# Performance work log

Measured on AMD Instinct MI355X. Metric: run time of the kernel, lower is better.

The kernel has to match this reference:

```python
import jax, jax.numpy as jnp
import numpy as np

D_MODEL = 1024
NUM_HEADS = 16
D_K = D_MODEL // NUM_HEADS
B, T = 2, 2048


def setup_inputs() -> dict:
    key = jax.random.key(0)
    k1, k2, k3 = jax.random.split(key, 3)
    scale = 1.0 / np.sqrt(D_MODEL)
    return {
        "x": jax.random.normal(k1, (B, T, D_MODEL), dtype=jnp.float32),
        "Wqkv": jax.random.normal(k2, (D_MODEL, 3 * D_MODEL), dtype=jnp.float32) * scale,
        "bqkv": jnp.zeros((3 * D_MODEL,), dtype=jnp.float32),
        "Wout": jax.random.normal(k3, (D_MODEL, D_MODEL), dtype=jnp.float32) * scale,
        "bout": jnp.zeros((D_MODEL,), dtype=jnp.float32),
    }


def reference(x, Wqkv, bqkv, Wout, bout):
    b, t, c = x.shape
    h, dk = NUM_HEADS, D_K
    qkv = x @ Wqkv + bqkv                      # [B,T,3C]
    q, k, v = jnp.split(qkv, 3, axis=-1)       # each [B,T,C]

    def split_heads(u):
        return u.reshape(b, t, h, dk).transpose(0, 2, 1, 3)  # [B,H,T,dk]

    q, k, v = split_heads(q), split_heads(k), split_heads(v)
    scores = jnp.einsum("bhqd,bhkd->bhqk", q, k) / jnp.sqrt(jnp.float32(dk))
    causal = jnp.tril(jnp.ones((t, t), dtype=bool))          # True = keep
    scores = jnp.where(causal, scores, -jnp.inf)
    attn = jax.nn.softmax(scores, axis=-1)
    out = jnp.einsum("bhqk,bhkd->bhqd", attn, v)             # [B,H,T,dk]
    concat = out.transpose(0, 2, 1, 3).reshape(b, t, c)
    return concat @ Wout + bout
```

## Files before the change

kernel.cpp:

```cpp
#include <hip/hip_runtime.h>
#include <hip/hip_bf16.h>

#define DEVI __device__ __forceinline__

typedef __attribute__((ext_vector_type(8))) short bf16x8;
typedef __attribute__((ext_vector_type(4))) float f32x4;

DEVI void load_lds16(const void* g, void* l) {
  __builtin_amdgcn_global_load_lds((const __attribute__((address_space(1))) void*)g,
                                   (__attribute__((address_space(3))) void*)l, 16, 0, 0);
}

DEVI short f32_to_bf16_bits(float f) {
  __hip_bfloat16 b = __float2bfloat16(f);
  return __builtin_bit_cast(short, b);
}

__global__ __launch_bounds__(256) void cvt_bf16_kernel(
    const float* __restrict__ in, __hip_bfloat16* __restrict__ out, int n4) {
  int i = blockIdx.x * 256 + threadIdx.x;
  if (i < n4) {
    float4 v = ((const float4*)in)[i];
    ushort4 o;
    o.x = (unsigned short)f32_to_bf16_bits(v.x);
    o.y = (unsigned short)f32_to_bf16_bits(v.y);
    o.z = (unsigned short)f32_to_bf16_bits(v.z);
    o.w = (unsigned short)f32_to_bf16_bits(v.w);
    ((ushort4*)out)[i] = o;
  }
}

__global__ __launch_bounds__(256) void transpose_bf16_kernel(
    const float* __restrict__ in, __hip_bfloat16* __restrict__ out, int K, int N) {
  __shared__ float tile[32][33];
  int tx = threadIdx.x, ty = threadIdx.y;
  int bx = blockIdx.x, by = blockIdx.y;
#pragma unroll
  for (int i = 0; i < 4; ++i) {
    int k = by * 32 + ty + i * 8;
    int n = bx * 32 + tx;
    tile[ty + i * 8][tx] = in[(size_t)k * N + n];
  }
  __syncthreads();
#pragma unroll
  for (int i = 0; i < 4; ++i) {
    int n = bx * 32 + ty + i * 8;
    int k = by * 32 + tx;
    out[(size_t)n * K + k] = __float2bfloat16(tile[tx][ty + i * 8]);
  }
}

template <int MODE>
__global__ __launch_bounds__(256) void gemm_bt_kernel(
    const __hip_bfloat16* __restrict__ A, const __hip_bfloat16* __restrict__ Bt,
    const float* __restrict__ bias, void* __restrict__ Cout,
    unsigned short* __restrict__ vt, int M, int N, int K) {
  __shared__ short As[128 * 64];
  __shared__ short Bs[128 * 64];
  const int tid = threadIdx.x;
  const int wid = tid >> 6, lane = tid & 63;
  const int bm = blockIdx.y, bn = blockIdx.x;
  const int row0 = bm * 128, col0 = bn * 128;
  const int wr = wid >> 1, wc = wid & 1;
  f32x4 acc[4][4] = {};

  for (int kt = 0; kt < K; kt += 64) {
    __syncthreads();
#pragma unroll
    for (int c = 0; c < 4; ++c) {
      int r = wid * 32 + c * 8 + (lane >> 3);
      int ss = (lane & 7) ^ (r & 7);
      load_lds16(A + (size_t)(row0 + r) * K + kt + ss * 8, As + (wid * 32 + c * 8) * 64);
      load_lds16(Bt + (size_t)(col0 + r) * K + kt + ss * 8, Bs + (wid * 32 + c * 8) * 64);
    }
    __syncthreads();
#pragma unroll
    for (int ks = 0; ks < 2; ++ks) {
      bf16x8 af[4], bf[4];
#pragma unroll
      for (int mi = 0; mi < 4; ++mi) {
        int r = wr * 64 + mi * 16 + (lane & 15);
        int sl = (ks * 4 + (lane >> 4)) ^ (r & 7);
        af[mi] = *(const bf16x8*)(As + r * 64 + sl * 8);
      }
#pragma unroll
      for (int ni = 0; ni < 4; ++ni) {
        int r = wc * 64 + ni * 16 + (lane & 15);
        int sl = (ks * 4 + (lane >> 4)) ^ (r & 7);
        bf[ni] = *(const bf16x8*)(Bs + r * 64 + sl * 8);
      }
#pragma unroll
      for (int mi = 0; mi < 4; ++mi)
#pragma unroll
        for (int ni = 0; ni < 4; ++ni)
          acc[mi][ni] = __builtin_amdgcn_mfma_f32_16x16x32_bf16(af[mi], bf[ni], acc[mi][ni], 0, 0, 0);
    }
  }
  const int crow0 = row0 + wr * 64, ccol0 = col0 + wc * 64;
#pragma unroll
  for (int ni = 0; ni < 4; ++ni) {
    int cc = ccol0 + ni * 16 + (lane & 15);
    float bv = bias[cc];
    if (MODE == 2 && cc >= 2048) {
      int dcol = cc - 2048;
      int hh = dcol >> 6, dl = dcol & 63;
#pragma unroll
      for (int mi = 0; mi < 4; ++mi) {
        int rr0 = crow0 + mi * 16 + (lane >> 4) * 4;
        int bI = rr0 >> 11, t0 = rr0 & 2047;
        ushort4 pk;
        pk.x = (unsigned short)f32_to_bf16_bits(acc[mi][ni][0] + bv);
        pk.y = (unsigned short)f32_to_bf16_bits(acc[mi][ni][1] + bv);
        pk.z = (unsigned short)f32_to_bf16_bits(acc[mi][ni][2] + bv);
        pk.w = (unsigned short)f32_to_bf16_bits(acc[mi][ni][3] + bv);
        *(ushort4*)(vt + ((size_t)(bI * 16 + hh) * 64 + dl) * 2048 + t0) = pk;
      }
    } else {
#pragma unroll
      for (int mi = 0; mi < 4; ++mi) {
#pragma unroll
        for (int r = 0; r < 4; ++r) {
          int rr = crow0 + mi * 16 + (lane >> 4) * 4 + r;
          float v = acc[mi][ni][r] + bv;
          if (MODE == 2)
            ((__hip_bfloat16*)Cout)[(size_t)rr * 2048 + cc] = __float2bfloat16(v);
          else
            ((float*)Cout)[(size_t)rr * N + cc] = v;
        }
      }
    }
  }
}

__global__ __launch_bounds__(256) void attn_kernel(
    const __hip_bfloat16* __restrict__ qk, const __hip_bfloat16* __restrict__ vt,
    __hip_bfloat16* __restrict__ concat) {
  const int bh = blockIdx.x;
  const int qb = blockIdx.y;
  const int b = bh >> 4, h = bh & 15;
  const int tid = threadIdx.x, wid = tid >> 6, lane = tid & 63;
  const size_t RS = 2048;
  const __hip_bfloat16* Qb = qk + (size_t)b * 2048 * RS + h * 64;
  const __hip_bfloat16* Kb = Qb + 1024;
  const __hip_bfloat16* Vh = vt + (size_t)bh * 64 * 2048;

  __shared__ short Ks[2][64 * 64];
  __shared__ short Vs[2][64 * 64];
  __shared__ short Ps[4][16 * 64];

  bf16x8 qf[2];
#pragma unroll
  for (int s = 0; s < 2; ++s)
    qf[s] = *(const bf16x8*)(Qb + (size_t)(qb * 64 + wid * 16 + (lane & 15)) * RS + s * 32 + (lane >> 4) * 8);

  f32x4 oacc[4] = {};
  float m_r[4], l_r[4];
#pragma unroll
  for (int r = 0; r < 4; ++r) { m_r[r] = -__builtin_inff(); l_r[r] = 0.f; }

#pragma unroll
  for (int c = 0; c < 2; ++c) {
    int r = wid * 16 + c * 8 + (lane >> 3);
    int ss = (lane & 7) ^ (r & 7);
    load_lds16(Kb + (size_t)r * RS + ss * 8, &Ks[0][(wid * 16 + c * 8) * 64]);
    load_lds16(Vh + (size_t)r * 2048 + ss * 8, &Vs[0][(wid * 16 + c * 8) * 64]);
  }
  int cur = 0;
  const float cs = 0.18033688f;

  for (int kt = 0; kt <= qb; ++kt) {
    __syncthreads();
    if (kt < qb) {
      int kn = kt + 1;
#pragma unroll
      for (int c = 0; c < 2; ++c) {
        int r = wid * 16 + c * 8 + (lane >> 3);
        int ss = (lane & 7) ^ (r & 7);
        load_lds16(Kb + (size_t)(kn * 64 + r) * RS + ss * 8, &Ks[cur ^ 1][(wid * 16 + c * 8) * 64]);
        load_lds16(Vh + (size_t)r * 2048 + kn * 64 + ss * 8, &Vs[cur ^ 1][(wid * 16 + c * 8) * 64]);
      }
    }

    f32x4 sacc[4] = {};
#pragma unroll
    for (int s = 0; s < 2; ++s) {
#pragma unroll
      for (int nt = 0; nt < 4; ++nt) {
        int r = nt * 16 + (lane & 15);
        int sl = (s * 4 + (lane >> 4)) ^ (r & 7);
        bf16x8 kf = *(const bf16x8*)(&Ks[cur][r * 64 + sl * 8]);
        sacc[nt] = __builtin_amdgcn_mfma_f32_16x16x32_bf16(qf[s], kf, sacc[nt], 0, 0, 0);
      }
    }

    const bool diag = (kt == qb);
#pragma unroll
    for (int r = 0; r < 4; ++r) {
      int qg = wid * 16 + (lane >> 4) * 4 + r;
      float rm = -3.0e38f;
#pragma unroll
      for (int nt = 0; nt < 4; ++nt) {
        float v = sacc[nt][r] * cs;
        if (diag) {
          int kg = nt * 16 + (lane & 15);
          v = (kg > qg) ? -1e30f : v;
        }
        sacc[nt][r] = v;
        rm = fmaxf(rm, v);
      }
#pragma unroll
      for (int off = 1; off < 16; off <<= 1) rm = fmaxf(rm, __shfl_xor(rm, off));
      float mn = fmaxf(m_r[r], rm);
      float al = exp2f(m_r[r] - mn);
      float rs = 0.f;
#pragma unroll
      for (int nt = 0; nt < 4; ++nt) {
        float p = exp2f(sacc[nt][r] - mn);
        sacc[nt][r] = p;
        rs += p;
      }
#pragma unroll
      for (int off = 1; off < 16; off <<= 1) rs += __shfl_xor(rs, off);
      l_r[r] = l_r[r] * al + rs;
      m_r[r] = mn;
#pragma unroll
      for (int dt = 0; dt < 4; ++dt) oacc[dt][r] *= al;
    }

#pragma unroll
    for (int nt = 0; nt < 4; ++nt)
#pragma unroll
      for (int r = 0; r < 4; ++r) {
        int q = (lane >> 4) * 4 + r;
        int key = nt * 16 + (lane & 15);
        int sl = (key >> 3) ^ (q & 7);
        Ps[wid][q * 64 + sl * 8 + (key & 7)] = f32_to_bf16_bits(sacc[nt][r]);
      }

#pragma unroll
    for (int s = 0; s < 2; ++s) {
      int q = lane & 15;
      int psl = (s * 4 + (lane >> 4)) ^ (q & 7);
      bf16x8 pf = *(const bf16x8*)(&Ps[wid][q * 64 + psl * 8]);
#pragma unroll
      for (int dt = 0; dt < 4; ++dt) {
        int d = dt * 16 + (lane & 15);
        int vsl = (s * 4 + (lane >> 4)) ^ (d & 7);
        bf16x8 vf = *(const bf16x8*)(&Vs[cur][d * 64 + vsl * 8]);
        oacc[dt] = __builtin_amdgcn_mfma_f32_16x16x32_bf16(pf, vf, oacc[dt], 0, 0, 0);
      }
    }
    cur ^= 1;
  }

  const size_t orow = (size_t)b * 2048;
#pragma unroll
  for (int dt = 0; dt < 4; ++dt)
#pragma unroll
    for (int r = 0; r < 4; ++r) {
      int qg = qb * 64 + wid * 16 + (lane >> 4) * 4 + r;
      float v = oacc[dt][r] / l_r[r];
      concat[(orow + qg) * 1024 + h * 64 + dt * 16 + (lane & 15)] = __float2bfloat16(v);
    }
}

extern "C" void kernel_launch(void* const* d_in, const int* in_sizes, int n_in,
                              void* d_out, int out_size, void* d_ws, size_t ws_size,
                              hipStream_t stream) {
  const float* x    = (const float*)d_in[0];
  const float* Wqkv = (const float*)d_in[1];
  const float* bqkv = (const float*)d_in[2];
  const float* Wout = (const float*)d_in[3];
  const float* bout = (const float*)d_in[4];
  float* out = (float*)d_out;

  char* ws = (char*)d_ws;
  __hip_bfloat16* xb    = (__hip_bfloat16*)(ws);
  __hip_bfloat16* cat   = (__hip_bfloat16*)(ws);
  __hip_bfloat16* WqkvT = (__hip_bfloat16*)(ws + 8388608);
  __hip_bfloat16* WoutT = (__hip_bfloat16*)(ws + 14680064);
  __hip_bfloat16* qkvqk = (__hip_bfloat16*)(ws + 16777216);
  __hip_bfloat16* vtb   = (__hip_bfloat16*)(ws + 33554432);

  cvt_bf16_kernel<<<dim3(4096), dim3(256), 0, stream>>>(x, xb, 4194304 / 4);
  transpose_bf16_kernel<<<dim3(3072 / 32, 1024 / 32), dim3(32, 8), 0, stream>>>(Wqkv, WqkvT, 1024, 3072);
  transpose_bf16_kernel<<<dim3(1024 / 32, 1024 / 32), dim3(32, 8), 0, stream>>>(Wout, WoutT, 1024, 1024);
  gemm_bt_kernel<2><<<dim3(3072 / 128, 4096 / 128), dim3(256), 0, stream>>>(
      xb, WqkvT, bqkv, (void*)qkvqk, (unsigned short*)vtb, 4096, 3072, 1024);
  attn_kernel<<<dim3(32, 32), dim3(256), 0, stream>>>(qkvqk, vtb, cat);
  gemm_bt_kernel<0><<<dim3(1024 / 128, 4096 / 128), dim3(256), 0, stream>>>(
      cat, WoutT, bout, (void*)out, nullptr, 4096, 1024, 1024);
}
```

Measured before the change: 228.2 us.

## Rework attention to 128-query tiles with 32x32 MFMA and register-resident P

Attention blocks now cover 128 query rows (32 per wave) instead of 64, halving the grid and sharing each K/V tile load across twice as many queries. Blocks are scheduled heaviest-first. The kernel uses 32x32x16 MFMAs with keys as the A operand, so the softmax row reduction needs only one cross-half shuffle. P is packed to bf16 in registers and exchanged via shuffles instead of a round trip through LDS. This cuts LDS traffic and shuffle overhead, but uses more registers per wave and leaves fewer blocks to fill the CUs.

After: 207.8 us. -8.9%, faster.

```diff
diff --git a/kernel.cpp b/kernel.cpp
--- a/kernel.cpp
+++ b/kernel.cpp
@@ -5,6 +5,7 @@
 
 typedef __attribute__((ext_vector_type(8))) short bf16x8;
 typedef __attribute__((ext_vector_type(4))) float f32x4;
+typedef __attribute__((ext_vector_type(16))) float f32x16;
 
 DEVI void load_lds16(const void* g, void* l) {
   __builtin_amdgcn_global_load_lds((const __attribute__((address_space(1))) void*)g,
@@ -14,6 +15,12 @@
 DEVI short f32_to_bf16_bits(float f) {
   __hip_bfloat16 b = __float2bfloat16(f);
   return __builtin_bit_cast(short, b);
+}
+
+DEVI unsigned pk_bf16(float lo, float hi) {
+  unsigned r;
+  asm("v_cvt_pk_bf16_f32 %0, %1, %2" : "=v"(r) : "v"(lo), "v"(hi));
+  return r;
 }
 
 __global__ __launch_bounds__(256) void cvt_bf16_kernel(
@@ -136,9 +143,12 @@
     const __hip_bfloat16* __restrict__ qk, const __hip_bfloat16* __restrict__ vt,
     __hip_bfloat16* __restrict__ concat) {
   const int bh = blockIdx.x;
-  const int qb = blockIdx.y;
+  const int jr = 15 - (int)blockIdx.y;
+  const int qb0 = jr * 128;
+  const int NT = 2 * jr + 2;
   const int b = bh >> 4, h = bh & 15;
   const int tid = threadIdx.x, wid = tid >> 6, lane = tid & 63;
+  const int ql = lane & 31, hl = lane >> 5;
   const size_t RS = 2048;
   const __hip_bfloat16* Qb = qk + (size_t)b * 2048 * RS + h * 64;
   const __hip_bfloat16* Kb = Qb + 1024;
@@ -146,17 +156,16 @@
 
   __shared__ short Ks[2][64 * 64];
   __shared__ short Vs[2][64 * 64];
-  __shared__ short Ps[4][16 * 64];
-
-  bf16x8 qf[2];
-#pragma unroll
-  for (int s = 0; s < 2; ++s)
-    qf[s] = *(const bf16x8*)(Qb + (size_t)(qb * 64 + wid * 16 + (lane & 15)) * RS + s * 32 + (lane >> 4) * 8);
-
-  f32x4 oacc[4] = {};
-  float m_r[4], l_r[4];
-#pragma unroll
-  for (int r = 0; r < 4; ++r) { m_r[r] = -__builtin_inff(); l_r[r] = 0.f; }
+
+  const int qrow = qb0 + wid * 32 + ql;
+  bf16x8 qf[4];
+#pragma unroll
+  for (int s = 0; s < 4; ++s)
+    qf[s] = *(const bf16x8*)(Qb + (size_t)qrow * RS + s * 16 + hl * 8);
+
+  f32x16 oacc[2] = {};
+  float m = -__builtin_inff(), l = 0.f;
+  const float cs = 0.18033688f;
 
 #pragma unroll
   for (int c = 0; c < 2; ++c) {
@@ -166,11 +175,11 @@
     load_lds16(Vh + (size_t)r * 2048 + ss * 8, &Vs[0][(wid * 16 + c * 8) * 64]);
   }
   int cur = 0;
-  const float cs = 0.18033688f;
-
-  for (int kt = 0; kt <= qb; ++kt) {
+  const int ktmax = (qb0 + 32 * wid + 31) >> 6;
+
+  for (int kt = 0; kt < NT; ++kt) {
     __syncthreads();
-    if (kt < qb) {
+    if (kt + 1 < NT) {
       int kn = kt + 1;
 #pragma unroll
       for (int c = 0; c < 2; ++c) {
@@ -180,87 +189,92 @@
         load_lds16(Vh + (size_t)r * 2048 + kn * 64 + ss * 8, &Vs[cur ^ 1][(wid * 16 + c * 8) * 64]);
       }
     }
-
-    f32x4 sacc[4] = {};
-#pragma unroll
-    for (int s = 0; s < 2; ++s) {
-#pragma unroll
-      for (int nt = 0; nt < 4; ++nt) {
-        int r = nt * 16 + (lane & 15);
-        int sl = (s * 4 + (lane >> 4)) ^ (r & 7);
-        bf16x8 kf = *(const bf16x8*)(&Ks[cur][r * 64 + sl * 8]);
-        sacc[nt] = __builtin_amdgcn_mfma_f32_16x16x32_bf16(qf[s], kf, sacc[nt], 0, 0, 0);
-      }
-    }
-
-    const bool diag = (kt == qb);
-#pragma unroll
-    for (int r = 0; r < 4; ++r) {
-      int qg = wid * 16 + (lane >> 4) * 4 + r;
+    if (kt <= ktmax) {
+      f32x16 sacc[2] = {};
+#pragma unroll
+      for (int s = 0; s < 4; ++s)
+#pragma unroll
+        for (int kb = 0; kb < 2; ++kb) {
+          int row = kb * 32 + ql;
+          int slot = (2 * s + hl) ^ (ql & 7);
+          bf16x8 kf = *(const bf16x8*)(&Ks[cur][row * 64 + slot * 8]);
+          sacc[kb] = __builtin_amdgcn_mfma_f32_32x32x16_bf16(kf, qf[s], sacc[kb], 0, 0, 0);
+        }
+      if (kt * 64 + 63 > qb0 + 32 * wid) {
+#pragma unroll
+        for (int kb = 0; kb < 2; ++kb)
+#pragma unroll
+          for (int r = 0; r < 16; ++r) {
+            int kg = kt * 64 + kb * 32 + (r & 3) + 8 * (r >> 2) + 4 * hl;
+            if (kg > qrow) sacc[kb][r] = -1e30f;
+          }
+      }
       float rm = -3.0e38f;
 #pragma unroll
-      for (int nt = 0; nt < 4; ++nt) {
-        float v = sacc[nt][r] * cs;
-        if (diag) {
-          int kg = nt * 16 + (lane & 15);
-          v = (kg > qg) ? -1e30f : v;
+      for (int kb = 0; kb < 2; ++kb)
+#pragma unroll
+        for (int r = 0; r < 16; ++r) rm = fmaxf(rm, sacc[kb][r]);
+      rm = fmaxf(rm, __shfl_xor(rm, 32));
+      float mn = fmaxf(m, rm);
+      float al = exp2f((m - mn) * cs);
+      float mcs = mn * cs;
+      float rs = 0.f;
+#pragma unroll
+      for (int kb = 0; kb < 2; ++kb)
+#pragma unroll
+        for (int r = 0; r < 16; ++r) {
+          float p = exp2f(fmaf(sacc[kb][r], cs, -mcs));
+          sacc[kb][r] = p;
+          rs += p;
         }
-        sacc[nt][r] = v;
-        rm = fmaxf(rm, v);
-      }
-#pragma unroll
-      for (int off = 1; off < 16; off <<= 1) rm = fmaxf(rm, __shfl_xor(rm, off));
-      float mn = fmaxf(m_r[r], rm);
-      float al = exp2f(m_r[r] - mn);
-      float rs = 0.f;
-#pragma unroll
-      for (int nt = 0; nt < 4; ++nt) {
-        float p = exp2f(sacc[nt][r] - mn);
-        sacc[nt][r] = p;
-        rs += p;
-      }
-#pragma unroll
-      for (int off = 1; off < 16; off <<= 1) rs += __shfl_xor(rs, off);
-      l_r[r] = l_r[r] * al + rs;
-      m_r[r] = mn;
-#pragma unroll
-      for (int dt = 0; dt < 4; ++dt) oacc[dt][r] *= al;
-    }
-
-#pragma unroll
-    for (int nt = 0; nt < 4; ++nt)
-#pragma unroll
-      for (int r = 0; r < 4; ++r) {
-        int q = (lane >> 4) * 4 + r;
-        int key = nt * 16 + (lane & 15);
-        int sl = (key >> 3) ^ (q & 7);
-        Ps[wid][q * 64 + sl * 8 + (key & 7)] = f32_to_bf16_bits(sacc[nt][r]);
-      }
-
-#pragma unroll
-    for (int s = 0; s < 2; ++s) {
-      int q = lane & 15;
-      int psl = (s * 4 + (lane >> 4)) ^ (q & 7);
-      bf16x8 pf = *(const bf16x8*)(&Ps[wid][q * 64 + psl * 8]);
-#pragma unroll
-      for (int dt = 0; dt < 4; ++dt) {
-        int d = dt * 16 + (lane & 15);
-        int vsl = (s * 4 + (lane >> 4)) ^ (d & 7);
-        bf16x8 vf = *(const bf16x8*)(&Vs[cur][d * 64 + vsl * 8]);
-        oacc[dt] = __builtin_amdgcn_mfma_f32_16x16x32_bf16(pf, vf, oacc[dt], 0, 0, 0);
+      rs += __shfl_xor(rs, 32);
+      l = l * al + rs;
+      m = mn;
+#pragma unroll
+      for (int db = 0; db < 2; ++db)
+#pragma unroll
+        for (int r = 0; r < 16; ++r) oacc[db][r] *= al;
+
+#pragma unroll
+      for (int kk = 0; kk < 4; ++kk) {
+        int kb = kk >> 1;
+        int be = 8 * (kk & 1);
+        unsigned x0 = pk_bf16(sacc[kb][be + 0], sacc[kb][be + 1]);
+        unsigned x1 = pk_bf16(sacc[kb][be + 2], sacc[kb][be + 3]);
+        unsigned y0 = pk_bf16(sacc[kb][be + 4], sacc[kb][be + 5]);
+        unsigned y1 = pk_bf16(sacc[kb][be + 6], sacc[kb][be + 7]);
+        unsigned x0p = __shfl_xor(x0, 32), x1p = __shfl_xor(x1, 32);
+        unsigned y0p = __shfl_xor(y0, 32), y1p = __shfl_xor(y1, 32);
+        union { unsigned u[4]; bf16x8 v; } pb;
+        pb.u[0] = hl ? y0p : x0;
+        pb.u[1] = hl ? y1p : x1;
+        pb.u[2] = hl ? y0 : x0p;
+        pb.u[3] = hl ? y1 : x1p;
+#pragma unroll
+        for (int db = 0; db < 2; ++db) {
+          int row = db * 32 + ql;
+          int slot = (2 * kk + hl) ^ (ql & 7);
+          bf16x8 vf = *(const bf16x8*)(&Vs[cur][row * 64 + slot * 8]);
+          oacc[db] = __builtin_amdgcn_mfma_f32_32x32x16_bf16(vf, pb.v, oacc[db], 0, 0, 0);
+        }
       }
     }
     cur ^= 1;
   }
 
-  const size_t orow = (size_t)b * 2048;
-#pragma unroll
-  for (int dt = 0; dt < 4; ++dt)
-#pragma unroll
-    for (int r = 0; r < 4; ++r) {
-      int qg = qb * 64 + wid * 16 + (lane >> 4) * 4 + r;
-      float v = oacc[dt][r] / l_r[r];
-      concat[(orow + qg) * 1024 + h * 64 + dt * 16 + (lane & 15)] = __float2bfloat16(v);
+  float rl = 1.0f / l;
+  const size_t orow = (size_t)b * 2048 + qrow;
+#pragma unroll
+  for (int db = 0; db < 2; ++db)
+#pragma unroll
+    for (int rr = 0; rr < 4; ++rr) {
+      int d0 = db * 32 + 8 * rr + 4 * hl;
+      ushort4 pkv;
+      pkv.x = (unsigned short)f32_to_bf16_bits(oacc[db][4 * rr + 0] * rl);
+      pkv.y = (unsigned short)f32_to_bf16_bits(oacc[db][4 * rr + 1] * rl);
+      pkv.z = (unsigned short)f32_to_bf16_bits(oacc[db][4 * rr + 2] * rl);
+      pkv.w = (unsigned short)f32_to_bf16_bits(oacc[db][4 * rr + 3] * rl);
+      *(ushort4*)(concat + orow * 1024 + h * 64 + d0) = pkv;
     }
 }
 
@@ -287,7 +301,7 @@
   transpose_bf16_kernel<<<dim3(1024 / 32, 1024 / 32), dim3(32, 8), 0, stream>>>(Wout, WoutT, 1024, 1024);
   gemm_bt_kernel<2><<<dim3(3072 / 128, 4096 / 128), dim3(256), 0, stream>>>(
       xb, WqkvT, bqkv, (void*)qkvqk, (unsigned short*)vtb, 4096, 3072, 1024);
-  attn_kernel<<<dim3(32, 32), dim3(256), 0, stream>>>(qkvqk, vtb, cat);
+  attn_kernel<<<dim3(32, 16), dim3(256), 0, stream>>>(qkvqk, vtb, cat);
   gemm_bt_kernel<0><<<dim3(1024 / 128, 4096 / 128), dim3(256), 0, stream>>>(
       cat, WoutT, bout, (void*)out, nullptr, 4096, 1024, 1024);
 }
```
